# Performance work log

Measured on AMD Instinct MI355X. Metric: run time of the kernel, lower is better.

Reference implementation:

```python
import jax, jax.numpy as jnp
import numpy as np

N_EMBD = 1024
N_HEAD = 16
HEAD_DIM = N_EMBD // N_HEAD
LN_EPS = 1e-5


def setup_inputs() -> dict:
    key = jax.random.key(0)
    ks = jax.random.split(key, 8)
    C = N_EMBD
    s = 0.02
    return {
        "x": jax.random.normal(ks[0], (2, 2048, C), dtype=jnp.float32),
        "ln1_g": jnp.ones((C,), jnp.float32),
        "ln1_b": jnp.zeros((C,), jnp.float32),
        "qkv_w": jax.random.normal(ks[1], (C, 3 * C), jnp.float32) * s,
        "qkv_b": jnp.zeros((3 * C,), jnp.float32),
        "out_w": jax.random.normal(ks[2], (C, C), jnp.float32) * s,
        "out_b": jnp.zeros((C,), jnp.float32),
        "ln2_g": jnp.ones((C,), jnp.float32),
        "ln2_b": jnp.zeros((C,), jnp.float32),
        "fc1_w": jax.random.normal(ks[3], (C, 4 * C), jnp.float32) * s,
        "fc1_b": jnp.zeros((4 * C,), jnp.float32),
        "fc2_w": jax.random.normal(ks[4], (4 * C, C), jnp.float32) * s,
        "fc2_b": jnp.zeros((C,), jnp.float32),
    }


def _layernorm(x, g, b):
    mu = jnp.mean(x, axis=-1, keepdims=True)
    var = jnp.var(x, axis=-1, keepdims=True)
    return (x - mu) * jax.lax.rsqrt(var + LN_EPS) * g + b


def reference(x, ln1_g, ln1_b, qkv_w, qkv_b, out_w, out_b,
              ln2_g, ln2_b, fc1_w, fc1_b, fc2_w, fc2_b):
    B, T, C = x.shape
    H, D = N_HEAD, HEAD_DIM

    # --- attention (pre-norm) ---
    h = _layernorm(x, ln1_g, ln1_b)
    qkv = h @ qkv_w + qkv_b                      # [B,T,3C]
    q, k, v = jnp.split(qkv, 3, axis=-1)
    q = q.reshape(B, T, H, D).transpose(0, 2, 1, 3)  # [B,H,T,D]
    k = k.reshape(B, T, H, D).transpose(0, 2, 1, 3)
    v = v.reshape(B, T, H, D).transpose(0, 2, 1, 3)

    attn = jnp.einsum('bhqd,bhkd->bhqk', q, k) / jnp.sqrt(jnp.float32(D))
    causal = jnp.tril(jnp.ones((T, T), bool))
    attn = jnp.where(causal, attn, -jnp.inf)
    attn = jax.nn.softmax(attn, axis=-1)
    o = jnp.einsum('bhqk,bhkd->bhqd', attn, v)   # [B,H,T,D]
    o = o.transpose(0, 2, 1, 3).reshape(B, T, C)
    x = x + (o @ out_w + out_b)

    # --- FFN (pre-norm) ---
    h = _layernorm(x, ln2_g, ln2_b)
    h = jax.nn.gelu(h @ fc1_w + fc1_b, approximate=False)
    x = x + (h @ fc2_w + fc2_b)
    return x
```

## Files before the change

### kernel.cpp

```cpp
#include <hip/hip_runtime.h>
#include <hip/hip_bf16.h>
#include <cstdint>

#define DEVI __device__ __forceinline__

typedef __attribute__((ext_vector_type(8))) short bf16x8;
typedef __attribute__((ext_vector_type(4))) float f32x4;

DEVI ushort f2bf(float f){
  union { float f; uint32_t u; } c; c.f = f;
  uint32_t u = c.u + 0x7fffu + ((c.u >> 16) & 1u);
  return (ushort)(u >> 16);
}

DEVI void gload_lds16(const void* g, void* l){
  __builtin_amdgcn_global_load_lds((const __attribute__((address_space(1))) void*)g,
                                   (__attribute__((address_space(3))) void*)l,
                                   16, 0, 0);
}

__global__ __launch_bounds__(256)
void transpose_cast(const float* __restrict__ in, ushort* __restrict__ out, int R, int C){
  __shared__ float tile[32][33];
  const int tx = threadIdx.x & 31, ty = threadIdx.x >> 5;
  const int bx = blockIdx.x * 32, by = blockIdx.y * 32;
  #pragma unroll
  for (int i = 0; i < 4; ++i)
    tile[ty + i*8][tx] = in[(size_t)(by + ty + i*8) * C + bx + tx];
  __syncthreads();
  #pragma unroll
  for (int i = 0; i < 4; ++i)
    out[(size_t)(bx + ty + i*8) * R + by + tx] = f2bf(tile[tx][ty + i*8]);
}

__global__ __launch_bounds__(256)
void ln_kernel(const float* __restrict__ x, const float* __restrict__ g,
               const float* __restrict__ b, ushort* __restrict__ out){
  const int row = blockIdx.x, tid = threadIdx.x;
  const float4 v = ((const float4*)(x + (size_t)row * 1024))[tid];
  float s  = v.x + v.y + v.z + v.w;
  float ss = v.x*v.x + v.y*v.y + v.z*v.z + v.w*v.w;
  #pragma unroll
  for (int off = 32; off > 0; off >>= 1){
    s  += __shfl_down(s,  off);
    ss += __shfl_down(ss, off);
  }
  __shared__ float red[8];
  const int wave = tid >> 6, lane = tid & 63;
  if (lane == 0){ red[wave] = s; red[4 + wave] = ss; }
  __syncthreads();
  s  = red[0] + red[1] + red[2] + red[3];
  ss = red[4] + red[5] + red[6] + red[7];
  const float mean = s * (1.0f/1024.0f);
  const float var  = ss * (1.0f/1024.0f) - mean*mean;
  const float rstd = rsqrtf(var + 1e-5f);
  const float4 gv = ((const float4*)g)[tid];
  const float4 bv = ((const float4*)b)[tid];
  ushort4 o;
  o.x = f2bf((v.x - mean) * rstd * gv.x + bv.x);
  o.y = f2bf((v.y - mean) * rstd * gv.y + bv.y);
  o.z = f2bf((v.z - mean) * rstd * gv.z + bv.z);
  o.w = f2bf((v.w - mean) * rstd * gv.w + bv.w);
  ((ushort4*)(out + (size_t)row * 1024))[tid] = o;
}

constexpr int BM = 128, BN = 128, BK = 32;
enum { EPI_QKV = 0, EPI_RES = 1, EPI_GELU = 2 };

template<int EPI>
__global__ __launch_bounds__(256, 2)
void gemm_bt(const ushort* __restrict__ A, const ushort* __restrict__ Bt,
             const float* __restrict__ bias, const float* __restrict__ resid,
             void* __restrict__ outp, int M, int N, int K)
{
  __shared__ ushort sA[BM*BK];
  __shared__ ushort sB[BN*BK];
  const int tid  = threadIdx.x;
  const int wave = tid >> 6, lane = tid & 63;
  const int l15 = lane & 15, g = lane >> 4;
  const int nbn = N / BN;
  const int mb = (blockIdx.x / nbn) * BM;
  const int nb = (blockIdx.x % nbn) * BN;
  const int wm = (wave >> 1) * 64, wn = (wave & 1) * 64;
  f32x4 acc[4][4] = {};
  const int arow = mb + (tid >> 2);
  const int brow = nb + (tid >> 2);
  const int kcol = (tid & 3) * 8;

  for (int kb = 0; kb < K; kb += BK){
    gload_lds16(A  + (size_t)arow      * K + kb + kcol, &sA[wave*512]);
    gload_lds16(A  + (size_t)(arow+64) * K + kb + kcol, &sA[2048 + wave*512]);
    gload_lds16(Bt + (size_t)brow      * K + kb + kcol, &sB[wave*512]);
    gload_lds16(Bt + (size_t)(brow+64) * K + kb + kcol, &sB[2048 + wave*512]);
    __syncthreads();
    bf16x8 af[4], bfv[4];
    const bf16x8* pA = (const bf16x8*)sA;
    const bf16x8* pB = (const bf16x8*)sB;
    #pragma unroll
    for (int i = 0; i < 4; ++i) af[i]  = pA[(wm + i*16 + l15)*4 + g];
    #pragma unroll
    for (int j = 0; j < 4; ++j) bfv[j] = pB[(wn + j*16 + l15)*4 + g];
    #pragma unroll
    for (int i = 0; i < 4; ++i)
      #pragma unroll
      for (int j = 0; j < 4; ++j)
        acc[i][j] = __builtin_amdgcn_mfma_f32_16x16x32_bf16(af[i], bfv[j], acc[i][j], 0, 0, 0);
    __syncthreads();
  }

  #pragma unroll
  for (int i = 0; i < 4; ++i){
    #pragma unroll
    for (int j = 0; j < 4; ++j){
      const int col = nb + wn + j*16 + l15;
      #pragma unroll
      for (int r = 0; r < 4; ++r){
        const int row = mb + wm + i*16 + g*4 + r;
        float vv = acc[i][j][r] + bias[col];
        if constexpr (EPI == EPI_RES){
          ((float*)outp)[(size_t)row * N + col] = vv + resid[(size_t)row * N + col];
        } else if constexpr (EPI == EPI_GELU){
          const float ge = 0.5f * vv * (1.0f + erff(vv * 0.70710678118f));
          ((ushort*)outp)[(size_t)row * N + col] = f2bf(ge);
        } else {
          const int which = col >> 10, c = col & 1023;
          const int head = c >> 6, d = c & 63;
          const int bb = row >> 11, t = row & 2047;
          ((ushort*)outp)[(size_t)which * 4194304 +
                          (((size_t)(bb*16 + head)) * 2048 + t) * 64 + d] = f2bf(vv);
        }
      }
    }
  }
}

__global__ __launch_bounds__(256, 2)
void attn_kernel(const ushort* __restrict__ Q, const ushort* __restrict__ K,
                 const ushort* __restrict__ V, ushort* __restrict__ O)
{
  constexpr int T = 2048, D = 64, LD = 72, NT = 32;
  __shared__ ushort sK[64*LD];
  __shared__ ushort sV[64*LD];
  __shared__ ushort sP[4][16*LD];
  const int tid = threadIdx.x, wave = tid >> 6, lane = tid & 63;
  const int l15 = lane & 15, g = lane >> 4;
  const int qtA = blockIdx.x;
  const int qtB = NT - 1 - qtA;
  const int bh = blockIdx.y;
  const size_t base = (size_t)bh * T * D;

  bf16x8 qfA[2], qfB[2];
  {
    const bf16x8* QA = (const bf16x8*)(Q + base + (size_t)(qtA*64 + wave*16 + l15) * D);
    qfA[0] = QA[g]; qfA[1] = QA[g + 4];
    const bf16x8* QB = (const bf16x8*)(Q + base + (size_t)(qtB*64 + wave*16 + l15) * D);
    qfB[0] = QB[g]; qfB[1] = QB[g + 4];
  }
  f32x4 oaA[4] = {}, oaB[4] = {};
  float mA[4], lA[4], mB[4], lB[4];
  #pragma unroll
  for (int r = 0; r < 4; ++r){ mA[r] = mB[r] = -1e30f; lA[r] = lB[r] = 0.f; }

  const int skey = tid >> 2, sd0 = (tid & 3) * 16;
  const int kp = tid & 31,  dv0 = (tid >> 5) * 8;

  auto tile_step = [&](int kt, int qt, const bf16x8* qf, f32x4* oa, float* m_r, float* l_r){
    f32x4 sf[4] = {};
    #pragma unroll
    for (int cf = 0; cf < 4; ++cf)
      #pragma unroll
      for (int kk = 0; kk < 2; ++kk){
        const bf16x8 kb = *(const bf16x8*)&sK[(cf*16 + l15)*LD + g*8 + kk*32];
        sf[cf] = __builtin_amdgcn_mfma_f32_16x16x32_bf16(qf[kk], kb, sf[cf], 0, 0, 0);
      }
    float p[4][4], rmax[4];
    const int qrow0 = qt*64 + wave*16 + g*4;
    const bool diag = (kt == qt);
    #pragma unroll
    for (int r = 0; r < 4; ++r) rmax[r] = -1e30f;
    #pragma unroll
    for (int cf = 0; cf < 4; ++cf)
      #pragma unroll
      for (int r = 0; r < 4; ++r){
        float s = sf[cf][r] * 0.125f;
        if (diag && (kt*64 + cf*16 + l15) > (qrow0 + r)) s = -1e30f;
        p[cf][r] = s;
        rmax[r] = fmaxf(rmax[r], s);
      }
    #pragma unroll
    for (int off = 1; off < 16; off <<= 1)
      #pragma unroll
      for (int r = 0; r < 4; ++r)
        rmax[r] = fmaxf(rmax[r], __shfl_xor(rmax[r], off));
    float alpha[4], lsum[4];
    #pragma unroll
    for (int r = 0; r < 4; ++r){
      const float mn = fmaxf(m_r[r], rmax[r]);
      alpha[r] = __expf(m_r[r] - mn);
      m_r[r] = mn;
      lsum[r] = 0.f;
    }
    #pragma unroll
    for (int cf = 0; cf < 4; ++cf)
      #pragma unroll
      for (int r = 0; r < 4; ++r){
        const float e = __expf(p[cf][r] - m_r[r]);
        p[cf][r] = e;
        lsum[r] += e;
      }
    #pragma unroll
    for (int off = 1; off < 16; off <<= 1)
      #pragma unroll
      for (int r = 0; r < 4; ++r)
        lsum[r] += __shfl_xor(lsum[r], off);
    #pragma unroll
    for (int r = 0; r < 4; ++r) l_r[r] = l_r[r]*alpha[r] + lsum[r];
    #pragma unroll
    for (int cf = 0; cf < 4; ++cf)
      #pragma unroll
      for (int r = 0; r < 4; ++r) oa[cf][r] *= alpha[r];

    uint32_t pk[16];
    #pragma unroll
    for (int cf = 0; cf < 4; ++cf)
      #pragma unroll
      for (int r = 0; r < 4; ++r){
        const float e = p[cf][r];
        const float o = __shfl_xor(e, 1);
        pk[cf*4 + r] = (uint32_t)f2bf(e) | ((uint32_t)f2bf(o) << 16);
      }
    if (!(lane & 1)){
      #pragma unroll
      for (int cf = 0; cf < 4; ++cf)
        #pragma unroll
        for (int r = 0; r < 4; ++r)
          *(uint32_t*)&sP[wave][(g*4 + r)*LD + cf*16 + l15] = pk[cf*4 + r];
    }
    bf16x8 pa[2];
    pa[0] = *(const bf16x8*)&sP[wave][l15*LD + g*8];
    pa[1] = *(const bf16x8*)&sP[wave][l15*LD + g*8 + 32];
    #pragma unroll
    for (int cf = 0; cf < 4; ++cf)
      #pragma unroll
      for (int kk = 0; kk < 2; ++kk){
        const bf16x8 vb = *(const bf16x8*)&sV[(cf*16 + l15)*LD + g*8 + kk*32];
        oa[cf] = __builtin_amdgcn_mfma_f32_16x16x32_bf16(pa[kk], vb, oa[cf], 0, 0, 0);
      }
  };

  for (int kt = 0; kt <= qtB; ++kt){
    const ushort* ks = K + base + (size_t)(kt*64 + skey) * D + sd0;
    *(bf16x8*)&sK[skey*LD + sd0]     = *(const bf16x8*)ks;
    *(bf16x8*)&sK[skey*LD + sd0 + 8] = *(const bf16x8*)(ks + 8);
    const ushort* vs = V + base + (size_t)(kt*64 + 2*kp) * D + dv0;
    const bf16x8 va = *(const bf16x8*)vs;
    const bf16x8 vb = *(const bf16x8*)(vs + D);
    #pragma unroll
    for (int j = 0; j < 8; ++j){
      const uint32_t pr = (uint32_t)(ushort)va[j] | ((uint32_t)(ushort)vb[j] << 16);
      *(uint32_t*)&sV[(dv0 + j)*LD + 2*kp] = pr;
    }
    __syncthreads();
    tile_step(kt, qtB, qfB, oaB, mB, lB);
    if (kt <= qtA) tile_step(kt, qtA, qfA, oaA, mA, lA);
    __syncthreads();
  }

  const int bb = bh >> 4, h = bh & 15;
  #pragma unroll
  for (int cf = 0; cf < 4; ++cf)
    #pragma unroll
    for (int r = 0; r < 4; ++r){
      const int rowB = qtB*64 + wave*16 + g*4 + r;
      O[((size_t)bb * T + rowB) * 1024 + h*64 + cf*16 + l15] = f2bf(oaB[cf][r] / lB[r]);
      const int rowA = qtA*64 + wave*16 + g*4 + r;
      O[((size_t)bb * T + rowA) * 1024 + h*64 + cf*16 + l15] = f2bf(oaA[cf][r] / lA[r]);
    }
}

extern "C" void kernel_launch(void* const* d_in, const int* in_sizes, int n_in,
                              void* d_out, int out_size, void* d_ws, size_t ws_size,
                              hipStream_t stream)
{
  const float* x     = (const float*)d_in[0];
  const float* ln1_g = (const float*)d_in[1];
  const float* ln1_b = (const float*)d_in[2];
  const float* qkv_w = (const float*)d_in[3];
  const float* qkv_b = (const float*)d_in[4];
  const float* out_w = (const float*)d_in[5];
  const float* out_b = (const float*)d_in[6];
  const float* ln2_g = (const float*)d_in[7];
  const float* ln2_b = (const float*)d_in[8];
  const float* fc1_w = (const float*)d_in[9];
  const float* fc1_b = (const float*)d_in[10];
  const float* fc2_w = (const float*)d_in[11];
  const float* fc2_b = (const float*)d_in[12];

  char* ws = (char*)d_ws;
  ushort* qkvwt = (ushort*)(ws + 0);
  ushort* outwt = (ushort*)(ws + 6291456);
  ushort* fc1wt = (ushort*)(ws + 8388608);
  ushort* fc2wt = (ushort*)(ws + 16777216);
  float*  x2    = (float*) (ws + 25165824);
  ushort* hbuf  = (ushort*)(ws + 41943040);
  ushort* qbuf  = (ushort*)(ws + 50331648);
  ushort* kbuf  = qbuf + 4194304;
  ushort* vbuf  = qbuf + 8388608;
  ushort* aout  = (ushort*)(ws + 75497472);
  ushort* h3    = (ushort*)(ws + 50331648);

  transpose_cast<<<dim3(96, 32),  256, 0, stream>>>(qkv_w, qkvwt, 1024, 3072);
  transpose_cast<<<dim3(32, 32),  256, 0, stream>>>(out_w, outwt, 1024, 1024);
  transpose_cast<<<dim3(128, 32), 256, 0, stream>>>(fc1_w, fc1wt, 1024, 4096);
  transpose_cast<<<dim3(32, 128), 256, 0, stream>>>(fc2_w, fc2wt, 4096, 1024);

  ln_kernel<<<4096, 256, 0, stream>>>(x, ln1_g, ln1_b, hbuf);
  gemm_bt<EPI_QKV><<<32*24, 256, 0, stream>>>(hbuf, qkvwt, qkv_b, nullptr, qbuf, 4096, 3072, 1024);
  attn_kernel<<<dim3(16, 32), 256, 0, stream>>>(qbuf, kbuf, vbuf, aout);
  gemm_bt<EPI_RES><<<32*8, 256, 0, stream>>>(aout, outwt, out_b, x, x2, 4096, 1024, 1024);
  ln_kernel<<<4096, 256, 0, stream>>>(x2, ln2_g, ln2_b, hbuf);
  gemm_bt<EPI_GELU><<<32*32, 256, 0, stream>>>(hbuf, fc1wt, fc1_b, nullptr, h3, 4096, 4096, 1024);
  gemm_bt<EPI_RES><<<32*8, 256, 0, stream>>>(h3, fc2wt, fc2_b, x2, (float*)d_out, 4096, 1024, 4096);
}
```

Measured before the change: 424.7 us.

## Split attention KV loop across two wave groups and merge softmax states

Doubles the attention block to 512 threads. The two 4-wave groups process alternating key tiles with separate K/V shared buffers, then merge their online-softmax states (m, l, partial O) through shared memory before writeout. This halves the serial KV loop length per block so more waves are available on the few blocks in the grid. It also folds the 1/sqrt(D) scale into exp2 and skips the mask check on non-diagonal tiles. In exchange it adds a shared-memory merge step, extra barriers and more LDS per block.

```diff
diff --git a/kernel.cpp b/kernel.cpp
--- a/kernel.cpp
+++ b/kernel.cpp
@@ -134,15 +134,19 @@
   }
 }
 
-__global__ __launch_bounds__(256, 2)
+__global__ __launch_bounds__(512, 4)
 void attn_kernel(const ushort* __restrict__ Q, const ushort* __restrict__ K,
                  const ushort* __restrict__ V, ushort* __restrict__ O)
 {
   constexpr int T = 2048, D = 64, LD = 72, NT = 32;
-  __shared__ ushort sK[64*LD];
-  __shared__ ushort sV[64*LD];
-  __shared__ ushort sP[4][16*LD];
+  constexpr float SC = 0.125f * 1.44269504f;
+  __shared__ ushort sK[2][64*LD];
+  __shared__ ushort sV[2][64*LD];
+  __shared__ ushort sP[8][16*LD];
+  __shared__ float  sMrg[4][64][25];
   const int tid = threadIdx.x, wave = tid >> 6, lane = tid & 63;
+  const int grp = wave >> 2;
+  const int wg  = wave & 3;
   const int l15 = lane & 15, g = lane >> 4;
   const int qtA = blockIdx.x;
   const int qtB = NT - 1 - qtA;
@@ -151,9 +155,9 @@
 
   bf16x8 qfA[2], qfB[2];
   {
-    const bf16x8* QA = (const bf16x8*)(Q + base + (size_t)(qtA*64 + wave*16 + l15) * D);
+    const bf16x8* QA = (const bf16x8*)(Q + base + (size_t)(qtA*64 + wg*16 + l15) * D);
     qfA[0] = QA[g]; qfA[1] = QA[g + 4];
-    const bf16x8* QB = (const bf16x8*)(Q + base + (size_t)(qtB*64 + wave*16 + l15) * D);
+    const bf16x8* QB = (const bf16x8*)(Q + base + (size_t)(qtB*64 + wg*16 + l15) * D);
     qfB[0] = QB[g]; qfB[1] = QB[g + 4];
   }
   f32x4 oaA[4] = {}, oaB[4] = {};
@@ -161,32 +165,44 @@
   #pragma unroll
   for (int r = 0; r < 4; ++r){ mA[r] = mB[r] = -1e30f; lA[r] = lB[r] = 0.f; }
 
-  const int skey = tid >> 2, sd0 = (tid & 3) * 16;
-  const int kp = tid & 31,  dv0 = (tid >> 5) * 8;
+  const int htid = tid & 255;
+  const int skey = htid >> 2, sd0 = (htid & 3) * 16;
+  const int kp = htid & 31,  dv0 = (htid >> 5) * 8;
 
   auto tile_step = [&](int kt, int qt, const bf16x8* qf, f32x4* oa, float* m_r, float* l_r){
+    const ushort* myK = sK[grp];
+    const ushort* myV = sV[grp];
     f32x4 sf[4] = {};
     #pragma unroll
     for (int cf = 0; cf < 4; ++cf)
       #pragma unroll
       for (int kk = 0; kk < 2; ++kk){
-        const bf16x8 kb = *(const bf16x8*)&sK[(cf*16 + l15)*LD + g*8 + kk*32];
+        const bf16x8 kb = *(const bf16x8*)&myK[(cf*16 + l15)*LD + g*8 + kk*32];
         sf[cf] = __builtin_amdgcn_mfma_f32_16x16x32_bf16(qf[kk], kb, sf[cf], 0, 0, 0);
       }
     float p[4][4], rmax[4];
-    const int qrow0 = qt*64 + wave*16 + g*4;
-    const bool diag = (kt == qt);
     #pragma unroll
     for (int r = 0; r < 4; ++r) rmax[r] = -1e30f;
-    #pragma unroll
-    for (int cf = 0; cf < 4; ++cf)
-      #pragma unroll
-      for (int r = 0; r < 4; ++r){
-        float s = sf[cf][r] * 0.125f;
-        if (diag && (kt*64 + cf*16 + l15) > (qrow0 + r)) s = -1e30f;
-        p[cf][r] = s;
-        rmax[r] = fmaxf(rmax[r], s);
-      }
+    if (kt == qt){
+      const int qrow0 = qt*64 + wg*16 + g*4;
+      #pragma unroll
+      for (int cf = 0; cf < 4; ++cf)
+        #pragma unroll
+        for (int r = 0; r < 4; ++r){
+          float s = sf[cf][r];
+          if ((kt*64 + cf*16 + l15) > (qrow0 + r)) s = -1e30f;
+          p[cf][r] = s;
+          rmax[r] = fmaxf(rmax[r], s);
+        }
+    } else {
+      #pragma unroll
+      for (int cf = 0; cf < 4; ++cf)
+        #pragma unroll
+        for (int r = 0; r < 4; ++r){
+          p[cf][r] = sf[cf][r];
+          rmax[r] = fmaxf(rmax[r], sf[cf][r]);
+        }
+    }
     #pragma unroll
     for (int off = 1; off < 16; off <<= 1)
       #pragma unroll
@@ -196,7 +212,7 @@
     #pragma unroll
     for (int r = 0; r < 4; ++r){
       const float mn = fmaxf(m_r[r], rmax[r]);
-      alpha[r] = __expf(m_r[r] - mn);
+      alpha[r] = exp2f((m_r[r] - mn) * SC);
       m_r[r] = mn;
       lsum[r] = 0.f;
     }
@@ -204,7 +220,7 @@
     for (int cf = 0; cf < 4; ++cf)
       #pragma unroll
       for (int r = 0; r < 4; ++r){
-        const float e = __expf(p[cf][r] - m_r[r]);
+        const float e = exp2f((p[cf][r] - m_r[r]) * SC);
         p[cf][r] = e;
         lsum[r] += e;
       }
@@ -243,39 +259,80 @@
     for (int cf = 0; cf < 4; ++cf)
       #pragma unroll
       for (int kk = 0; kk < 2; ++kk){
-        const bf16x8 vb = *(const bf16x8*)&sV[(cf*16 + l15)*LD + g*8 + kk*32];
+        const bf16x8 vb = *(const bf16x8*)&myV[(cf*16 + l15)*LD + g*8 + kk*32];
         oa[cf] = __builtin_amdgcn_mfma_f32_16x16x32_bf16(pa[kk], vb, oa[cf], 0, 0, 0);
       }
   };
 
-  for (int kt = 0; kt <= qtB; ++kt){
-    const ushort* ks = K + base + (size_t)(kt*64 + skey) * D + sd0;
-    *(bf16x8*)&sK[skey*LD + sd0]     = *(const bf16x8*)ks;
-    *(bf16x8*)&sK[skey*LD + sd0 + 8] = *(const bf16x8*)(ks + 8);
-    const ushort* vs = V + base + (size_t)(kt*64 + 2*kp) * D + dv0;
-    const bf16x8 va = *(const bf16x8*)vs;
-    const bf16x8 vb = *(const bf16x8*)(vs + D);
-    #pragma unroll
-    for (int j = 0; j < 8; ++j){
-      const uint32_t pr = (uint32_t)(ushort)va[j] | ((uint32_t)(ushort)vb[j] << 16);
-      *(uint32_t*)&sV[(dv0 + j)*LD + 2*kp] = pr;
-    }
-    __syncthreads();
-    tile_step(kt, qtB, qfB, oaB, mB, lB);
-    if (kt <= qtA) tile_step(kt, qtA, qfA, oaA, mA, lA);
-    __syncthreads();
-  }
-
-  const int bb = bh >> 4, h = bh & 15;
-  #pragma unroll
-  for (int cf = 0; cf < 4; ++cf)
-    #pragma unroll
-    for (int r = 0; r < 4; ++r){
-      const int rowB = qtB*64 + wave*16 + g*4 + r;
-      O[((size_t)bb * T + rowB) * 1024 + h*64 + cf*16 + l15] = f2bf(oaB[cf][r] / lB[r]);
-      const int rowA = qtA*64 + wave*16 + g*4 + r;
-      O[((size_t)bb * T + rowA) * 1024 + h*64 + cf*16 + l15] = f2bf(oaA[cf][r] / lA[r]);
-    }
+  for (int i = 0; 2*i <= qtB; ++i){
+    const int myt = 2*i + grp;
+    if (myt <= qtB){
+      const ushort* ks = K + base + (size_t)(myt*64 + skey) * D + sd0;
+      *(bf16x8*)&sK[grp][skey*LD + sd0]     = *(const bf16x8*)ks;
+      *(bf16x8*)&sK[grp][skey*LD + sd0 + 8] = *(const bf16x8*)(ks + 8);
+      const ushort* vs = V + base + (size_t)(myt*64 + 2*kp) * D + dv0;
+      const bf16x8 va = *(const bf16x8*)vs;
+      const bf16x8 vb = *(const bf16x8*)(vs + D);
+      #pragma unroll
+      for (int j = 0; j < 8; ++j){
+        const uint32_t pr = (uint32_t)(ushort)va[j] | ((uint32_t)(ushort)vb[j] << 16);
+        *(uint32_t*)&sV[grp][(dv0 + j)*LD + 2*kp] = pr;
+      }
+    }
+    __syncthreads();
+    if (myt <= qtB){
+      tile_step(myt, qtB, qfB, oaB, mB, lB);
+      if (myt <= qtA) tile_step(myt, qtA, qfA, oaA, mA, lA);
+    }
+    __syncthreads();
+  }
+
+  #pragma unroll
+  for (int t = 0; t < 2; ++t){
+    float* m_r = t ? mA : mB;
+    float* l_r = t ? lA : lB;
+    f32x4* oa  = t ? oaA : oaB;
+    if (grp == 1){
+      #pragma unroll
+      for (int r = 0; r < 4; ++r){ sMrg[wg][lane][r] = m_r[r]; sMrg[wg][lane][4+r] = l_r[r]; }
+      #pragma unroll
+      for (int cf = 0; cf < 4; ++cf)
+        #pragma unroll
+        for (int r = 0; r < 4; ++r) sMrg[wg][lane][8 + cf*4 + r] = oa[cf][r];
+    }
+    __syncthreads();
+    if (grp == 0){
+      float aE[4], aO[4];
+      #pragma unroll
+      for (int r = 0; r < 4; ++r){
+        const float mO = sMrg[wg][lane][r], lO = sMrg[wg][lane][4+r];
+        const float mn = fmaxf(m_r[r], mO);
+        aE[r] = exp2f((m_r[r] - mn) * SC);
+        aO[r] = exp2f((mO - mn) * SC);
+        l_r[r] = l_r[r]*aE[r] + lO*aO[r];
+        m_r[r] = mn;
+      }
+      #pragma unroll
+      for (int cf = 0; cf < 4; ++cf)
+        #pragma unroll
+        for (int r = 0; r < 4; ++r)
+          oa[cf][r] = oa[cf][r]*aE[r] + sMrg[wg][lane][8 + cf*4 + r]*aO[r];
+    }
+    __syncthreads();
+  }
+
+  if (grp == 0){
+    const int bb = bh >> 4, h = bh & 15;
+    #pragma unroll
+    for (int cf = 0; cf < 4; ++cf)
+      #pragma unroll
+      for (int r = 0; r < 4; ++r){
+        const int rowB = qtB*64 + wg*16 + g*4 + r;
+        O[((size_t)bb * T + rowB) * 1024 + h*64 + cf*16 + l15] = f2bf(oaB[cf][r] / lB[r]);
+        const int rowA = qtA*64 + wg*16 + g*4 + r;
+        O[((size_t)bb * T + rowA) * 1024 + h*64 + cf*16 + l15] = f2bf(oaA[cf][r] / lA[r]);
+      }
+  }
 }
 
 extern "C" void kernel_launch(void* const* d_in, const int* in_sizes, int n_in,
@@ -316,7 +373,7 @@
 
   ln_kernel<<<4096, 256, 0, stream>>>(x, ln1_g, ln1_b, hbuf);
   gemm_bt<EPI_QKV><<<32*24, 256, 0, stream>>>(hbuf, qkvwt, qkv_b, nullptr, qbuf, 4096, 3072, 1024);
-  attn_kernel<<<dim3(16, 32), 256, 0, stream>>>(qbuf, kbuf, vbuf, aout);
+  attn_kernel<<<dim3(16, 32), 512, 0, stream>>>(qbuf, kbuf, vbuf, aout);
   gemm_bt<EPI_RES><<<32*8, 256, 0, stream>>>(aout, outwt, out_b, x, x2, 4096, 1024, 1024);
   ln_kernel<<<4096, 256, 0, stream>>>(x2, ln2_g, ln2_b, hbuf);
   gemm_bt<EPI_GELU><<<32*32, 256, 0, stream>>>(hbuf, fc1wt, fc1_b, nullptr, h3, 4096, 4096, 1024);
```

Result: slower. 483.6 us (+13.9%).

## Use narrower N tiles for C-output GEMMs and remap workgroups across XCDs

Applied to the files above, without the earlier changes.

Templates the GEMM on its N tile width so the out-projection and fc2 GEMMs (N=1024) use 128x64 tiles, doubling their grid from 256 to 512 workgroups to better fill the 256 CUs. It also remaps blockIdx so consecutive logical tiles land on the same XCD (blockIdx&7 chunking), aiming for better L2 reuse of shared A/B rows. Narrower tiles lower arithmetic intensity per block and add A-tile reloads.

```diff
diff --git a/kernel.cpp b/kernel.cpp
--- a/kernel.cpp
+++ b/kernel.cpp
@@ -64,25 +64,28 @@
   ((ushort4*)(out + (size_t)row * 1024))[tid] = o;
 }
 
-constexpr int BM = 128, BN = 128, BK = 32;
+constexpr int BM = 128, BK = 32;
 enum { EPI_QKV = 0, EPI_RES = 1, EPI_GELU = 2 };
 
-template<int EPI>
+template<int EPI, int BNT>
 __global__ __launch_bounds__(256, 2)
 void gemm_bt(const ushort* __restrict__ A, const ushort* __restrict__ Bt,
              const float* __restrict__ bias, const float* __restrict__ resid,
              void* __restrict__ outp, int M, int N, int K)
 {
+  constexpr int NJ = BNT / 32;
   __shared__ ushort sA[BM*BK];
-  __shared__ ushort sB[BN*BK];
+  __shared__ ushort sB[BNT*BK];
   const int tid  = threadIdx.x;
   const int wave = tid >> 6, lane = tid & 63;
   const int l15 = lane & 15, g = lane >> 4;
-  const int nbn = N / BN;
-  const int mb = (blockIdx.x / nbn) * BM;
-  const int nb = (blockIdx.x % nbn) * BN;
-  const int wm = (wave >> 1) * 64, wn = (wave & 1) * 64;
-  f32x4 acc[4][4] = {};
+  const int nbn = N / BNT;
+  const int nwg = gridDim.x;
+  const int wg  = (blockIdx.x & 7) * (nwg >> 3) + (blockIdx.x >> 3);
+  const int mb = (wg / nbn) * BM;
+  const int nb = (wg % nbn) * BNT;
+  const int wm = (wave >> 1) * 64, wn = (wave & 1) * (BNT/2);
+  f32x4 acc[4][NJ] = {};
   const int arow = mb + (tid >> 2);
   const int brow = nb + (tid >> 2);
   const int kcol = (tid & 3) * 8;
@@ -91,19 +94,20 @@
     gload_lds16(A  + (size_t)arow      * K + kb + kcol, &sA[wave*512]);
     gload_lds16(A  + (size_t)(arow+64) * K + kb + kcol, &sA[2048 + wave*512]);
     gload_lds16(Bt + (size_t)brow      * K + kb + kcol, &sB[wave*512]);
-    gload_lds16(Bt + (size_t)(brow+64) * K + kb + kcol, &sB[2048 + wave*512]);
+    if constexpr (BNT == 128)
+      gload_lds16(Bt + (size_t)(brow+64) * K + kb + kcol, &sB[2048 + wave*512]);
     __syncthreads();
-    bf16x8 af[4], bfv[4];
+    bf16x8 af[4], bfv[NJ];
     const bf16x8* pA = (const bf16x8*)sA;
     const bf16x8* pB = (const bf16x8*)sB;
     #pragma unroll
     for (int i = 0; i < 4; ++i) af[i]  = pA[(wm + i*16 + l15)*4 + g];
     #pragma unroll
-    for (int j = 0; j < 4; ++j) bfv[j] = pB[(wn + j*16 + l15)*4 + g];
+    for (int j = 0; j < NJ; ++j) bfv[j] = pB[(wn + j*16 + l15)*4 + g];
     #pragma unroll
     for (int i = 0; i < 4; ++i)
       #pragma unroll
-      for (int j = 0; j < 4; ++j)
+      for (int j = 0; j < NJ; ++j)
         acc[i][j] = __builtin_amdgcn_mfma_f32_16x16x32_bf16(af[i], bfv[j], acc[i][j], 0, 0, 0);
     __syncthreads();
   }
@@ -111,7 +115,7 @@
   #pragma unroll
   for (int i = 0; i < 4; ++i){
     #pragma unroll
-    for (int j = 0; j < 4; ++j){
+    for (int j = 0; j < NJ; ++j){
       const int col = nb + wn + j*16 + l15;
       #pragma unroll
       for (int r = 0; r < 4; ++r){
@@ -315,10 +319,10 @@
   transpose_cast<<<dim3(32, 128), 256, 0, stream>>>(fc2_w, fc2wt, 4096, 1024);
 
   ln_kernel<<<4096, 256, 0, stream>>>(x, ln1_g, ln1_b, hbuf);
-  gemm_bt<EPI_QKV><<<32*24, 256, 0, stream>>>(hbuf, qkvwt, qkv_b, nullptr, qbuf, 4096, 3072, 1024);
+  gemm_bt<EPI_QKV,128><<<32*24, 256, 0, stream>>>(hbuf, qkvwt, qkv_b, nullptr, qbuf, 4096, 3072, 1024);
   attn_kernel<<<dim3(16, 32), 256, 0, stream>>>(qbuf, kbuf, vbuf, aout);
-  gemm_bt<EPI_RES><<<32*8, 256, 0, stream>>>(aout, outwt, out_b, x, x2, 4096, 1024, 1024);
+  gemm_bt<EPI_RES,64><<<32*16, 256, 0, stream>>>(aout, outwt, out_b, x, x2, 4096, 1024, 1024);
   ln_kernel<<<4096, 256, 0, stream>>>(x2, ln2_g, ln2_b, hbuf);
-  gemm_bt<EPI_GELU><<<32*32, 256, 0, stream>>>(hbuf, fc1wt, fc1_b, nullptr, h3, 4096, 4096, 1024);
-  gemm_bt<EPI_RES><<<32*8, 256, 0, stream>>>(h3, fc2wt, fc2_b, x2, (float*)d_out, 4096, 1024, 4096);
-}
+  gemm_bt<EPI_GELU,128><<<32*32, 256, 0, stream>>>(hbuf, fc1wt, fc1_b, nullptr, h3, 4096, 4096, 1024);
+  gemm_bt<EPI_RES,64><<<32*16, 256, 0, stream>>>(h3, fc2wt, fc2_b, x2, (float*)d_out, 4096, 1024, 4096);
+}
```

Result: faster. 407.7 us (-4.0%).
